# Kernel tuning notes

Measured on AMD Instinct MI355X. Metric: run time of the kernel, lower is better.

The kernel has to match this reference:

```python
import jax, jax.numpy as jnp
import numpy as np
import math

B, S, HID, NH = 4, 2048, 512, 8
DH = HID // NH
ALPHA = 1.33
N_ITER = 50  # bisection iterations (entmax default)


def entmax_bisect(X, alpha=ALPHA, n_iter=N_ITER):
    """entmax-bisect over the last axis (Peters et al.), faithful to the entmax lib."""
    inv = 1.0 / (alpha - 1.0)
    Xa = X * (alpha - 1.0)
    d = X.shape[-1]
    max_val = jnp.max(Xa, axis=-1, keepdims=True)
    tau_lo = max_val - 1.0
    tau_hi = max_val - (1.0 / d) ** (alpha - 1.0)
    f_lo = jnp.sum(jnp.clip(Xa - tau_lo, 0.0) ** inv, axis=-1, keepdims=True) - 1.0
    dm0 = tau_hi - tau_lo

    def body(carry, _):
        tau_lo, dm = carry
        dm = dm * 0.5
        tau_m = tau_lo + dm
        p_m = jnp.clip(Xa - tau_m, 0.0) ** inv
        f_m = jnp.sum(p_m, axis=-1, keepdims=True) - 1.0
        tau_lo = jnp.where(f_m * f_lo >= 0, tau_m, tau_lo)
        return (tau_lo, dm), None

    (tau_lo, _), _ = jax.lax.scan(body, (tau_lo, dm0), None, length=n_iter)
    p = jnp.clip(Xa - tau_lo, 0.0) ** inv
    return p / jnp.sum(p, axis=-1, keepdims=True)


def setup_inputs() -> dict:
    key = jax.random.key(0)
    ks = jax.random.split(key, 5)
    w = lambda k: jax.random.normal(k, (HID, HID), dtype=jnp.float32) * 0.02
    return {
        "hidden_states": jax.random.normal(ks[0], (B, S, HID), dtype=jnp.float32),
        "Wq": w(ks[1]), "bq": jnp.zeros((HID,), jnp.float32),
        "Wk": w(ks[2]), "bk": jnp.zeros((HID,), jnp.float32),
        "Wv": w(ks[3]), "bv": jnp.zeros((HID,), jnp.float32),
        "Wo": w(ks[4]), "bo": jnp.zeros((HID,), jnp.float32),
    }


def reference(hidden_states, Wq, bq, Wk, bk, Wv, bv, Wo, bo):
    # Linear projections (torch Linear: x @ W.T + b)
    def proj(x, W, b):
        y = jnp.einsum('bsh,oh->bso', x, W) + b
        # [B,S,NH,DH] -> [B,NH,S,DH]
        return y.reshape(B, S, NH, DH).transpose(0, 2, 1, 3)

    q = proj(hidden_states, Wq, bq)
    k = proj(hidden_states, Wk, bk)
    v = proj(hidden_states, Wv, bv)

    scores = jnp.einsum('bhqd,bhkd->bhqk', q, k) / math.sqrt(DH)  # [B,NH,S,S]
    probs = entmax_bisect(scores)                                 # entmax-1.33 over keys
    ctx = jnp.einsum('bhqk,bhkd->bhqd', probs, v)                 # [B,NH,S,DH]
    ctx = ctx.transpose(0, 2, 1, 3).reshape(B, S, HID)
    out = jnp.einsum('bsh,oh->bso', ctx, Wo) + bo
    return out  # vis=False, dropout=0 (eval)
```

## Files before the change

kernel.cpp:

```cpp
#include <hip/hip_runtime.h>
#include <math.h>

#define S_LEN 2048
#define HIDDIM 512
#define NHEAD 8
#define DHEAD 64
#define NBH 32
#define MTOT 8192

__device__ __forceinline__ float fast_exp2(float x) { return __builtin_amdgcn_exp2f(x); }
__device__ __forceinline__ float fast_log2(float x) { return __builtin_amdgcn_logf(x); }
__device__ __forceinline__ float powclip(float x, float pinv) {
    return fast_exp2(fast_log2(fmaxf(x, 0.f)) * pinv);
}

__global__ __launch_bounds__(256) void gemm_xwt(
    const float* __restrict__ X, const float* __restrict__ W,
    const float* __restrict__ bias, float* __restrict__ out,
    int mode, float scale)
{
    __shared__ float Xs[16][68];
    __shared__ float Ws[16][68];

    const int m0 = blockIdx.x * 64;
    const int n0 = blockIdx.y * 64;
    const int t  = threadIdx.x;
    const int tx = t & 15;
    const int ty = t >> 4;
    const int lrow = t >> 2;
    const int lk0  = (t & 3) << 2;

    float acc[4][4];
#pragma unroll
    for (int i = 0; i < 4; ++i)
#pragma unroll
        for (int j = 0; j < 4; ++j) acc[i][j] = 0.f;

    for (int kt = 0; kt < HIDDIM; kt += 16) {
        float4 xv = *(const float4*)&X[(size_t)(m0 + lrow) * HIDDIM + kt + lk0];
        float4 wv = *(const float4*)&W[(size_t)(n0 + lrow) * HIDDIM + kt + lk0];
        __syncthreads();
        Xs[lk0 + 0][lrow] = xv.x; Xs[lk0 + 1][lrow] = xv.y;
        Xs[lk0 + 2][lrow] = xv.z; Xs[lk0 + 3][lrow] = xv.w;
        Ws[lk0 + 0][lrow] = wv.x; Ws[lk0 + 1][lrow] = wv.y;
        Ws[lk0 + 2][lrow] = wv.z; Ws[lk0 + 3][lrow] = wv.w;
        __syncthreads();
#pragma unroll
        for (int kk = 0; kk < 16; ++kk) {
            float4 a = *(const float4*)&Xs[kk][ty << 2];
            float4 b = *(const float4*)&Ws[kk][tx << 2];
            float av[4] = {a.x, a.y, a.z, a.w};
            float bv[4] = {b.x, b.y, b.z, b.w};
#pragma unroll
            for (int i = 0; i < 4; ++i)
#pragma unroll
                for (int j = 0; j < 4; ++j) acc[i][j] += av[i] * bv[j];
        }
    }

#pragma unroll
    for (int i = 0; i < 4; ++i) {
        const int m  = m0 + (ty << 2) + i;
        const int bb = m >> 11;
        const int ss = m & 2047;
#pragma unroll
        for (int j = 0; j < 4; ++j) {
            const int n = n0 + (tx << 2) + j;
            const float v = (acc[i][j] + bias[n]) * scale;
            size_t idx;
            if (mode == 0) {
                idx = (size_t)m * HIDDIM + n;
            } else {
                const int h = n >> 6, d = n & 63;
                if (mode == 1)
                    idx = ((size_t)(bb * NHEAD + h) * S_LEN + ss) * DHEAD + d;
                else
                    idx = ((size_t)(bb * NHEAD + h) * DHEAD + d) * S_LEN + ss;
            }
            out[idx] = v;
        }
    }
}

__global__ __launch_bounds__(256) void attn_entmax(
    const float* __restrict__ Q,
    const float* __restrict__ Kt,
    const float* __restrict__ V,
    float* __restrict__ CTX,
    float pinv, float dm0)
{
    __shared__ float Qs[16][64];
    __shared__ float P[16][2052];
    __shared__ float rowsum[16];

    const int bh = blockIdx.x >> 7;
    const int q0 = (blockIdx.x & 127) << 4;
    const int t  = threadIdx.x;

    {
        const int r = t >> 4;
        const int d = (t & 15) << 2;
        *(float4*)&Qs[r][d] =
            *(const float4*)&Q[((size_t)bh * S_LEN + q0 + r) * DHEAD + d];
    }
    __syncthreads();

    const int w  = t >> 6;
    const int tc = t & 63;

    float sc[4][32];
#pragma unroll
    for (int i = 0; i < 4; ++i)
#pragma unroll
        for (int j = 0; j < 32; ++j) sc[i][j] = 0.f;

    const float* KtB = Kt + (size_t)bh * DHEAD * S_LEN;

#pragma unroll
    for (int kb = 0; kb < 8; ++kb) {
        const int kbase = (kb << 8) + (tc << 2);
        for (int dc = 0; dc < 16; ++dc) {
            const float* kp = KtB + (size_t)(dc << 2) * S_LEN + kbase;
            float4 k0 = *(const float4*)(kp);
            float4 k1 = *(const float4*)(kp + S_LEN);
            float4 k2 = *(const float4*)(kp + 2 * S_LEN);
            float4 k3 = *(const float4*)(kp + 3 * S_LEN);
#pragma unroll
            for (int i = 0; i < 4; ++i) {
                float4 q = *(const float4*)&Qs[(w << 2) + i][dc << 2];
                sc[i][(kb << 2) + 0] += q.x * k0.x + q.y * k1.x + q.z * k2.x + q.w * k3.x;
                sc[i][(kb << 2) + 1] += q.x * k0.y + q.y * k1.y + q.z * k2.y + q.w * k3.y;
                sc[i][(kb << 2) + 2] += q.x * k0.z + q.y * k1.z + q.z * k2.z + q.w * k3.z;
                sc[i][(kb << 2) + 3] += q.x * k0.w + q.y * k1.w + q.z * k2.w + q.w * k3.w;
            }
        }
    }

    float tau[4], flo[4];
    float dm = dm0;
#pragma unroll
    for (int i = 0; i < 4; ++i) {
        float m = sc[i][0];
#pragma unroll
        for (int j = 1; j < 32; ++j) m = fmaxf(m, sc[i][j]);
#pragma unroll
        for (int o = 32; o > 0; o >>= 1) m = fmaxf(m, __shfl_xor(m, o, 64));
        tau[i] = m - 1.0f;
    }
    {
        float ss[4] = {0.f, 0.f, 0.f, 0.f};
#pragma unroll
        for (int j = 0; j < 32; ++j)
#pragma unroll
            for (int i = 0; i < 4; ++i)
                ss[i] += powclip(sc[i][j] - tau[i], pinv);
#pragma unroll
        for (int i = 0; i < 4; ++i) {
#pragma unroll
            for (int o = 32; o > 0; o >>= 1) ss[i] += __shfl_xor(ss[i], o, 64);
            flo[i] = ss[i] - 1.0f;
        }
    }
    for (int it = 0; it < 32; ++it) {
        dm *= 0.5f;
        float tm[4], ss[4];
#pragma unroll
        for (int i = 0; i < 4; ++i) { tm[i] = tau[i] + dm; ss[i] = 0.f; }
#pragma unroll
        for (int j = 0; j < 32; ++j)
#pragma unroll
            for (int i = 0; i < 4; ++i)
                ss[i] += powclip(sc[i][j] - tm[i], pinv);
#pragma unroll
        for (int i = 0; i < 4; ++i) {
#pragma unroll
            for (int o = 32; o > 0; o >>= 1) ss[i] += __shfl_xor(ss[i], o, 64);
            if ((ss[i] - 1.0f) * flo[i] >= 0.f) tau[i] = tm[i];
        }
    }

#pragma unroll
    for (int i = 0; i < 4; ++i) {
        float s = 0.f;
#pragma unroll
        for (int j = 0; j < 32; ++j) {
            float p = powclip(sc[i][j] - tau[i], pinv);
            sc[i][j] = p;
            s += p;
        }
#pragma unroll
        for (int o = 32; o > 0; o >>= 1) s += __shfl_xor(s, o, 64);
#pragma unroll
        for (int kb = 0; kb < 8; ++kb) {
            float4 pw = make_float4(sc[i][(kb << 2) + 0], sc[i][(kb << 2) + 1],
                                    sc[i][(kb << 2) + 2], sc[i][(kb << 2) + 3]);
            *(float4*)&P[(w << 2) + i][(kb << 8) + (tc << 2)] = pw;
        }
        if (tc == 0) rowsum[(w << 2) + i] = s;
    }
    __syncthreads();

    const int r2 = t >> 4;
    const int dq = (t & 15) << 2;
    const float* VB = V + (size_t)bh * S_LEN * DHEAD;
    float ax = 0.f, ay = 0.f, az = 0.f, aw = 0.f;
    for (int k = 0; k < S_LEN; k += 4) {
        float4 p4 = *(const float4*)&P[r2][k];
        const float* vp = VB + (size_t)k * DHEAD + dq;
        float4 v0 = *(const float4*)(vp);
        float4 v1 = *(const float4*)(vp + DHEAD);
        float4 v2 = *(const float4*)(vp + 2 * DHEAD);
        float4 v3 = *(const float4*)(vp + 3 * DHEAD);
        ax += p4.x * v0.x + p4.y * v1.x + p4.z * v2.x + p4.w * v3.x;
        ay += p4.x * v0.y + p4.y * v1.y + p4.z * v2.y + p4.w * v3.y;
        az += p4.x * v0.z + p4.y * v1.z + p4.z * v2.z + p4.w * v3.z;
        aw += p4.x * v0.w + p4.y * v1.w + p4.z * v2.w + p4.w * v3.w;
    }
    const float rsc = 1.0f / rowsum[r2];
    const int b = bh >> 3, h = bh & 7;
    float4 o = make_float4(ax * rsc, ay * rsc, az * rsc, aw * rsc);
    *(float4*)&CTX[((size_t)b * S_LEN + q0 + r2) * HIDDIM + (h << 6) + dq] = o;
}

extern "C" void kernel_launch(void* const* d_in, const int* in_sizes, int n_in,
                              void* d_out, int out_size, void* d_ws, size_t ws_size,
                              hipStream_t stream)
{
    const float* hs = (const float*)d_in[0];
    const float* Wq = (const float*)d_in[1];
    const float* bq = (const float*)d_in[2];
    const float* Wk = (const float*)d_in[3];
    const float* bk = (const float*)d_in[4];
    const float* Wv = (const float*)d_in[5];
    const float* bv = (const float*)d_in[6];
    const float* Wo = (const float*)d_in[7];
    const float* bo = (const float*)d_in[8];
    float* out = (float*)d_out;

    const size_t per = (size_t)NBH * S_LEN * DHEAD;
    float* Qb  = (float*)d_ws;
    float* Ktb = Qb  + per;
    float* Vb  = Ktb + per;
    float* CTX = Vb  + per;

    const double am1d  = 1.33 - 1.0;
    const float qscale = (float)(am1d / 8.0);
    const float pinv   = (float)(1.0 / am1d);
    const float dm0    = (float)(1.0 - exp2(-11.0 * am1d));

    dim3 gp(MTOT / 64, HIDDIM / 64);
    gemm_xwt<<<gp, 256, 0, stream>>>(hs, Wq, bq, Qb,  1, qscale);
    gemm_xwt<<<gp, 256, 0, stream>>>(hs, Wk, bk, Ktb, 2, 1.0f);
    gemm_xwt<<<gp, 256, 0, stream>>>(hs, Wv, bv, Vb,  1, 1.0f);
    attn_entmax<<<dim3(NBH * (S_LEN / 16)), 256, 0, stream>>>(Qb, Ktb, Vb, CTX, pinv, dm0);
    gemm_xwt<<<gp, 256, 0, stream>>>(CTX, Wo, bo, out, 0, 1.0f);
}
```

Baseline: 4.441 ms.

## Halve rows per wave, cut bisection iterations, store P in fp16, transpose V

Doubles the attention block to 512 threads so each wave owns 2 query rows instead of 4, which cuts register pressure and lets more waves run per CU. The bisection loop goes from 32 to 22 iterations and drops the f_lo computation, using a sign test of sum >= 1 instead. The probability tile is stored in shared memory as fp16, halving LDS use, and V is now written transposed so the PV loop reads contiguous keys per head dimension. Fewer iterations and fp16 probabilities reduce the precision of tau and the output, and the sum >= 1 test assumes f_lo is never positive.

```diff
diff --git a/kernel.cpp b/kernel.cpp
--- a/kernel.cpp
+++ b/kernel.cpp
@@ -7,6 +7,8 @@
 #define DHEAD 64
 #define NBH 32
 #define MTOT 8192
+
+typedef _Float16 half4 __attribute__((ext_vector_type(4)));
 
 __device__ __forceinline__ float fast_exp2(float x) { return __builtin_amdgcn_exp2f(x); }
 __device__ __forceinline__ float fast_log2(float x) { return __builtin_amdgcn_logf(x); }
@@ -82,22 +84,22 @@
     }
 }
 
-__global__ __launch_bounds__(256) void attn_entmax(
+__global__ __launch_bounds__(512, 3) void attn_entmax(
     const float* __restrict__ Q,
     const float* __restrict__ Kt,
-    const float* __restrict__ V,
+    const float* __restrict__ Vt,
     float* __restrict__ CTX,
     float pinv, float dm0)
 {
     __shared__ float Qs[16][64];
-    __shared__ float P[16][2052];
+    __shared__ _Float16 P[16][2052];
     __shared__ float rowsum[16];
 
     const int bh = blockIdx.x >> 7;
     const int q0 = (blockIdx.x & 127) << 4;
     const int t  = threadIdx.x;
 
-    {
+    if (t < 256) {
         const int r = t >> 4;
         const int d = (t & 15) << 2;
         *(float4*)&Qs[r][d] =
@@ -107,10 +109,11 @@
 
     const int w  = t >> 6;
     const int tc = t & 63;
-
-    float sc[4][32];
-#pragma unroll
-    for (int i = 0; i < 4; ++i)
+    const int r0 = w << 1;
+
+    float sc[2][32];
+#pragma unroll
+    for (int i = 0; i < 2; ++i)
 #pragma unroll
         for (int j = 0; j < 32; ++j) sc[i][j] = 0.f;
 
@@ -126,8 +129,8 @@
             float4 k2 = *(const float4*)(kp + 2 * S_LEN);
             float4 k3 = *(const float4*)(kp + 3 * S_LEN);
 #pragma unroll
-            for (int i = 0; i < 4; ++i) {
-                float4 q = *(const float4*)&Qs[(w << 2) + i][dc << 2];
+            for (int i = 0; i < 2; ++i) {
+                float4 q = *(const float4*)&Qs[r0 + i][dc << 2];
                 sc[i][(kb << 2) + 0] += q.x * k0.x + q.y * k1.x + q.z * k2.x + q.w * k3.x;
                 sc[i][(kb << 2) + 1] += q.x * k0.y + q.y * k1.y + q.z * k2.y + q.w * k3.y;
                 sc[i][(kb << 2) + 2] += q.x * k0.z + q.y * k1.z + q.z * k2.z + q.w * k3.z;
@@ -136,10 +139,9 @@
         }
     }
 
-    float tau[4], flo[4];
-    float dm = dm0;
-#pragma unroll
-    for (int i = 0; i < 4; ++i) {
+    float tau[2];
+#pragma unroll
+    for (int i = 0; i < 2; ++i) {
         float m = sc[i][0];
 #pragma unroll
         for (int j = 1; j < 32; ++j) m = fmaxf(m, sc[i][j]);
@@ -147,79 +149,64 @@
         for (int o = 32; o > 0; o >>= 1) m = fmaxf(m, __shfl_xor(m, o, 64));
         tau[i] = m - 1.0f;
     }
-    {
-        float ss[4] = {0.f, 0.f, 0.f, 0.f};
-#pragma unroll
-        for (int j = 0; j < 32; ++j)
-#pragma unroll
-            for (int i = 0; i < 4; ++i)
-                ss[i] += powclip(sc[i][j] - tau[i], pinv);
-#pragma unroll
-        for (int i = 0; i < 4; ++i) {
-#pragma unroll
-            for (int o = 32; o > 0; o >>= 1) ss[i] += __shfl_xor(ss[i], o, 64);
-            flo[i] = ss[i] - 1.0f;
-        }
-    }
-    for (int it = 0; it < 32; ++it) {
+    float dm = dm0;
+    for (int it = 0; it < 22; ++it) {
         dm *= 0.5f;
-        float tm[4], ss[4];
-#pragma unroll
-        for (int i = 0; i < 4; ++i) { tm[i] = tau[i] + dm; ss[i] = 0.f; }
-#pragma unroll
-        for (int j = 0; j < 32; ++j)
-#pragma unroll
-            for (int i = 0; i < 4; ++i)
-                ss[i] += powclip(sc[i][j] - tm[i], pinv);
-#pragma unroll
-        for (int i = 0; i < 4; ++i) {
-#pragma unroll
-            for (int o = 32; o > 0; o >>= 1) ss[i] += __shfl_xor(ss[i], o, 64);
-            if ((ss[i] - 1.0f) * flo[i] >= 0.f) tau[i] = tm[i];
-        }
-    }
-
-#pragma unroll
-    for (int i = 0; i < 4; ++i) {
+        const float t0 = tau[0] + dm, t1 = tau[1] + dm;
+        float s0 = 0.f, s1 = 0.f;
+#pragma unroll
+        for (int j = 0; j < 32; ++j) {
+            s0 += powclip(sc[0][j] - t0, pinv);
+            s1 += powclip(sc[1][j] - t1, pinv);
+        }
+#pragma unroll
+        for (int o = 32; o > 0; o >>= 1) {
+            s0 += __shfl_xor(s0, o, 64);
+            s1 += __shfl_xor(s1, o, 64);
+        }
+        if (s0 >= 1.0f) tau[0] = t0;
+        if (s1 >= 1.0f) tau[1] = t1;
+    }
+
+#pragma unroll
+    for (int i = 0; i < 2; ++i) {
         float s = 0.f;
 #pragma unroll
-        for (int j = 0; j < 32; ++j) {
-            float p = powclip(sc[i][j] - tau[i], pinv);
-            sc[i][j] = p;
-            s += p;
+        for (int kb = 0; kb < 8; ++kb) {
+            half4 hv;
+#pragma unroll
+            for (int c = 0; c < 4; ++c) {
+                float p = powclip(sc[i][(kb << 2) + c] - tau[i], pinv);
+                s += p;
+                hv[c] = (_Float16)p;
+            }
+            *(half4*)&P[r0 + i][(kb << 8) + (tc << 2)] = hv;
         }
 #pragma unroll
         for (int o = 32; o > 0; o >>= 1) s += __shfl_xor(s, o, 64);
-#pragma unroll
-        for (int kb = 0; kb < 8; ++kb) {
-            float4 pw = make_float4(sc[i][(kb << 2) + 0], sc[i][(kb << 2) + 1],
-                                    sc[i][(kb << 2) + 2], sc[i][(kb << 2) + 3]);
-            *(float4*)&P[(w << 2) + i][(kb << 8) + (tc << 2)] = pw;
-        }
-        if (tc == 0) rowsum[(w << 2) + i] = s;
+        if (tc == 0) rowsum[r0 + i] = s;
     }
     __syncthreads();
 
-    const int r2 = t >> 4;
-    const int dq = (t & 15) << 2;
-    const float* VB = V + (size_t)bh * S_LEN * DHEAD;
-    float ax = 0.f, ay = 0.f, az = 0.f, aw = 0.f;
+    const int l   = t & 63;
+    const int row = l >> 2;
+    const int d   = (w << 3) + ((l & 3) << 1);
+    const float* v0 = Vt + ((size_t)bh * DHEAD + d) * S_LEN;
+    const float* v1 = v0 + S_LEN;
+    float a0 = 0.f, a1 = 0.f;
     for (int k = 0; k < S_LEN; k += 4) {
-        float4 p4 = *(const float4*)&P[r2][k];
-        const float* vp = VB + (size_t)k * DHEAD + dq;
-        float4 v0 = *(const float4*)(vp);
-        float4 v1 = *(const float4*)(vp + DHEAD);
-        float4 v2 = *(const float4*)(vp + 2 * DHEAD);
-        float4 v3 = *(const float4*)(vp + 3 * DHEAD);
-        ax += p4.x * v0.x + p4.y * v1.x + p4.z * v2.x + p4.w * v3.x;
-        ay += p4.x * v0.y + p4.y * v1.y + p4.z * v2.y + p4.w * v3.y;
-        az += p4.x * v0.z + p4.y * v1.z + p4.z * v2.z + p4.w * v3.z;
-        aw += p4.x * v0.w + p4.y * v1.w + p4.z * v2.w + p4.w * v3.w;
-    }
-    const float rsc = 1.0f / rowsum[r2];
+        half4 ph = *(const half4*)&P[row][k];
+        float4 x0 = *(const float4*)&v0[k];
+        float4 x1 = *(const float4*)&v1[k];
+        const float p0 = (float)ph[0], p1 = (float)ph[1];
+        const float p2 = (float)ph[2], p3 = (float)ph[3];
+        a0 += p0 * x0.x + p1 * x0.y + p2 * x0.z + p3 * x0.w;
+        a1 += p0 * x1.x + p1 * x1.y + p2 * x1.z + p3 * x1.w;
+    }
+    const float rsc = 1.0f / rowsum[row];
     const int b = bh >> 3, h = bh & 7;
-    float4 o = make_float4(ax * rsc, ay * rsc, az * rsc, aw * rsc);
-    *(float4*)&CTX[((size_t)b * S_LEN + q0 + r2) * HIDDIM + (h << 6) + dq] = o;
+    float2 o = make_float2(a0 * rsc, a1 * rsc);
+    *(float2*)&CTX[((size_t)b * S_LEN + q0 + row) * HIDDIM + (h << 6) + d] = o;
 }
 
 extern "C" void kernel_launch(void* const* d_in, const int* in_sizes, int n_in,
@@ -240,8 +227,8 @@
     const size_t per = (size_t)NBH * S_LEN * DHEAD;
     float* Qb  = (float*)d_ws;
     float* Ktb = Qb  + per;
-    float* Vb  = Ktb + per;
-    float* CTX = Vb  + per;
+    float* Vtb = Ktb + per;
+    float* CTX = Vtb + per;
 
     const double am1d  = 1.33 - 1.0;
     const float qscale = (float)(am1d / 8.0);
@@ -251,7 +238,7 @@
     dim3 gp(MTOT / 64, HIDDIM / 64);
     gemm_xwt<<<gp, 256, 0, stream>>>(hs, Wq, bq, Qb,  1, qscale);
     gemm_xwt<<<gp, 256, 0, stream>>>(hs, Wk, bk, Ktb, 2, 1.0f);
-    gemm_xwt<<<gp, 256, 0, stream>>>(hs, Wv, bv, Vb,  1, 1.0f);
-    attn_entmax<<<dim3(NBH * (S_LEN / 16)), 256, 0, stream>>>(Qb, Ktb, Vb, CTX, pinv, dm0);
+    gemm_xwt<<<gp, 256, 0, stream>>>(hs, Wv, bv, Vtb, 2, 1.0f);
+    attn_entmax<<<dim3(NBH * (S_LEN / 16)), 512, 0, stream>>>(Qb, Ktb, Vtb, CTX, pinv, dm0);
     gemm_xwt<<<gp, 256, 0, stream>>>(CTX, Wo, bo, out, 0, 1.0f);
 }
```

Result: slower. 7.521 ms (+69.4%).
